# Optimization experiments

Hardware: AMD Instinct MI355X
Metric: run time of the kernel (lower is better)

The kernel has to match this reference:

```python
import jax, jax.numpy as jnp
import numpy as np

EMBED_DIM = 512
NUM_HEADS = 8
HEAD_DIM = EMBED_DIM // NUM_HEADS


def setup_inputs() -> dict:
    key = jax.random.key(0)
    k1, k2, k3, k4, k5, k6 = jax.random.split(key, 6)
    B, S, D = 2, 4096, EMBED_DIM
    scale = 1.0 / np.sqrt(D)
    return {
        "inputs": jax.random.normal(k1, (B, S, D), dtype=jnp.float32),
        "Wq": jax.random.normal(k2, (D, D), dtype=jnp.float32) * scale,
        "Wk": jax.random.normal(k3, (D, D), dtype=jnp.float32) * scale,
        "Wv": jax.random.normal(k4, (D, D), dtype=jnp.float32) * scale,
        "Wc": jax.random.normal(k5, (D, D), dtype=jnp.float32) * scale,
        "bc": jax.random.normal(k6, (D,), dtype=jnp.float32) * 0.01,
    }


def reference(inputs, Wq, Wk, Wv, Wc, bc):
    B, S, D = inputs.shape
    H, Hd = NUM_HEADS, HEAD_DIM

    def split_heads(x):
        # [B,S,D] -> [B,H,S,Hd]
        return x.reshape(B, S, H, Hd).transpose(0, 2, 1, 3)

    # nn.Linear applies x @ W.T
    q = split_heads(inputs @ Wq.T).astype(jnp.float32)
    k = split_heads(inputs @ Wk.T).astype(jnp.float32)
    v = split_heads(inputs @ Wv.T).astype(jnp.float32)

    scores = jnp.einsum("bhqd,bhkd->bhqk", q, k) / np.sqrt(Hd).astype(jnp.float32)
    weights = jax.nn.softmax(scores, axis=-1)
    attended = jnp.einsum("bhqk,bhkd->bhqd", weights, v).astype(inputs.dtype)
    attended = attended.transpose(0, 2, 1, 3).reshape(B, S, D)
    return attended @ Wc.T + bc
```

## Files before the change

### kernel.cpp

```cpp
#include <hip/hip_runtime.h>
#include <cstdint>
#include <cstddef>

typedef _Float16 half_t;
typedef half_t h8 __attribute__((ext_vector_type(8)));
typedef half_t h4 __attribute__((ext_vector_type(4)));
typedef float f4 __attribute__((ext_vector_type(4)));
typedef unsigned int u32;

static constexpr int S_LEN  = 4096;
static constexpr int DMODEL = 512;
static constexpr int NH     = 8;
static constexpr int HD     = 64;
static constexpr int BATCH  = 2;
static constexpr int MTOK   = BATCH * S_LEN;

#define QSCALE 0.18033688011112043f

__device__ __forceinline__ void g2lds16(const void* g, void* l) {
    __builtin_amdgcn_global_load_lds(
        (const __attribute__((address_space(1))) u32*)(uintptr_t)g,
        (__attribute__((address_space(3))) u32*)(u32)(uintptr_t)l,
        16, 0, 0);
}

__device__ __forceinline__ f4 mfma16(h8 a, h8 b, f4 c) {
    return __builtin_amdgcn_mfma_f32_16x16x32_f16(a, b, c, 0, 0, 0);
}

__global__ void cvt_x(const float* __restrict__ in, half_t* __restrict__ out) {
    int i = (blockIdx.x * 256 + threadIdx.x) * 8;
    const float4* p = (const float4*)(in + i);
    float4 a = p[0], b = p[1];
    h8 h;
    h[0]=(half_t)a.x; h[1]=(half_t)a.y; h[2]=(half_t)a.z; h[3]=(half_t)a.w;
    h[4]=(half_t)b.x; h[5]=(half_t)b.y; h[6]=(half_t)b.z; h[7]=(half_t)b.w;
    *(h8*)(out + i) = h;
}

__global__ void cvt_w(const float* __restrict__ w0, const float* __restrict__ w1,
                      const float* __restrict__ w2, const float* __restrict__ w3,
                      half_t* __restrict__ o0, half_t* __restrict__ o1,
                      half_t* __restrict__ o2, half_t* __restrict__ o3) {
    int y = blockIdx.y;
    const float* in = (y==0) ? w0 : (y==1) ? w1 : (y==2) ? w2 : w3;
    half_t* out     = (y==0) ? o0 : (y==1) ? o1 : (y==2) ? o2 : o3;
    float s = (y==0) ? QSCALE : 1.0f;
    int i = (blockIdx.x * 256 + threadIdx.x) * 8;
    const float4* p = (const float4*)(in + i);
    float4 a = p[0], b = p[1];
    h8 h;
    h[0]=(half_t)(a.x*s); h[1]=(half_t)(a.y*s); h[2]=(half_t)(a.z*s); h[3]=(half_t)(a.w*s);
    h[4]=(half_t)(b.x*s); h[5]=(half_t)(b.y*s); h[6]=(half_t)(b.z*s); h[7]=(half_t)(b.w*s);
    *(h8*)(out + i) = h;
}

__device__ __forceinline__ void gemm_core(const half_t* __restrict__ A,
                                          const half_t* __restrict__ B,
                                          int m0, int n0, int Kdim,
                                          half_t* As, half_t* Bs,
                                          f4 (&acc)[4][4]) {
    const int tid  = threadIdx.x;
    const int lane = tid & 63;
    const int w    = tid >> 6;
    const int quad = lane >> 4;
    const int low  = lane & 15;
    const int wr   = (w >> 1) * 64;
    const int wc   = (w & 1) * 64;

    f4 zero = {0.f, 0.f, 0.f, 0.f};
    #pragma unroll
    for (int i = 0; i < 4; ++i)
        #pragma unroll
        for (int j = 0; j < 4; ++j) acc[i][j] = zero;

    for (int kk = 0; kk < Kdim; kk += 32) {
        __syncthreads();
        #pragma unroll
        for (int it = 0; it < 2; ++it) {
            int c = tid + 256 * it;
            int row = c >> 2, cs = c & 3;
            int gc = cs ^ ((row >> 1) & 3);
            g2lds16(A + (size_t)(m0 + row) * Kdim + kk + gc * 8, As + c * 8);
        }
        #pragma unroll
        for (int it = 0; it < 2; ++it) {
            int c = tid + 256 * it;
            int row = c >> 2, cs = c & 3;
            int gc = cs ^ ((row >> 1) & 3);
            g2lds16(B + (size_t)(n0 + row) * Kdim + kk + gc * 8, Bs + c * 8);
        }
        __syncthreads();

        h8 af[4], bf[4];
        #pragma unroll
        for (int i = 0; i < 4; ++i) {
            int r = wr + i * 16 + low;
            af[i] = *(const h8*)(As + r * 32 + (quad ^ ((r >> 1) & 3)) * 8);
        }
        #pragma unroll
        for (int j = 0; j < 4; ++j) {
            int r = wc + j * 16 + low;
            bf[j] = *(const h8*)(Bs + r * 32 + (quad ^ ((r >> 1) & 3)) * 8);
        }
        #pragma unroll
        for (int i = 0; i < 4; ++i)
            #pragma unroll
            for (int j = 0; j < 4; ++j)
                acc[i][j] = mfma16(af[i], bf[j], acc[i][j]);
    }
}

__global__ __launch_bounds__(256) void gemm_qkv(
    const half_t* __restrict__ X,
    const half_t* __restrict__ Wq, const half_t* __restrict__ Wk, const half_t* __restrict__ Wv,
    half_t* __restrict__ Q, half_t* __restrict__ K, half_t* __restrict__ V) {
    __shared__ half_t As[128 * 32];
    __shared__ half_t Bs[128 * 32];
    const int z = blockIdx.z;
    const half_t* W = (z == 0) ? Wq : (z == 1) ? Wk : Wv;
    half_t* O       = (z == 0) ? Q  : (z == 1) ? K  : V;

    const int m0 = blockIdx.y * 128;
    const int n0 = blockIdx.x * 128;
    f4 acc[4][4];
    gemm_core(X, W, m0, n0, DMODEL, As, Bs, acc);

    const int lane = threadIdx.x & 63;
    const int w    = threadIdx.x >> 6;
    const int quad = lane >> 4, low = lane & 15;
    const int wr = (w >> 1) * 64, wc = (w & 1) * 64;

    #pragma unroll
    for (int i = 0; i < 4; ++i) {
        int mb = m0 + wr + i * 16 + quad * 4;
        #pragma unroll
        for (int j = 0; j < 4; ++j) {
            int n = n0 + wc + j * 16 + low;
            int h = n >> 6, d = n & 63;
            #pragma unroll
            for (int r = 0; r < 4; ++r) {
                int m = mb + r;
                int b = m >> 12, s = m & 4095;
                size_t idx = (((size_t)(b * NH + h) << 12) + s) * 64 + d;
                O[idx] = (half_t)acc[i][j][r];
            }
        }
    }
}

__global__ __launch_bounds__(256) void gemm_out(
    const half_t* __restrict__ A, const half_t* __restrict__ W,
    const float* __restrict__ bias, float* __restrict__ out) {
    __shared__ half_t As[128 * 32];
    __shared__ half_t Bs[128 * 32];
    const int m0 = blockIdx.y * 128;
    const int n0 = blockIdx.x * 128;
    f4 acc[4][4];
    gemm_core(A, W, m0, n0, DMODEL, As, Bs, acc);

    const int lane = threadIdx.x & 63;
    const int w    = threadIdx.x >> 6;
    const int quad = lane >> 4, low = lane & 15;
    const int wr = (w >> 1) * 64, wc = (w & 1) * 64;

    #pragma unroll
    for (int i = 0; i < 4; ++i) {
        int mb = m0 + wr + i * 16 + quad * 4;
        #pragma unroll
        for (int j = 0; j < 4; ++j) {
            int n = n0 + wc + j * 16 + low;
            float bv = bias[n];
            #pragma unroll
            for (int r = 0; r < 4; ++r)
                out[(size_t)(mb + r) * DMODEL + n] = acc[i][j][r] + bv;
        }
    }
}

__global__ void transpose_v(const half_t* __restrict__ in, half_t* __restrict__ out) {
    int bh = blockIdx.y;
    int s  = blockIdx.x * 256 + threadIdx.x;
    const half_t* ip = in + ((size_t)bh << 18) + (size_t)s * 64;
    h8 v[8];
    #pragma unroll
    for (int c = 0; c < 8; ++c) v[c] = *(const h8*)(ip + c * 8);
    half_t* op = out + ((size_t)bh << 18) + s;
    #pragma unroll
    for (int d = 0; d < 64; ++d) op[(size_t)d * S_LEN] = v[d >> 3][d & 7];
}

__global__ __launch_bounds__(256, 2) void flash_attn(
    const half_t* __restrict__ Q,
    const half_t* __restrict__ K,
    const half_t* __restrict__ V,
    half_t* __restrict__ Oa) {
    __shared__ half_t Ks[128 * 64];
    __shared__ half_t Vs[64 * 128];
    __shared__ half_t Ps[4 * 32 * 32];

    const int tid  = threadIdx.x;
    const int lane = tid & 63;
    const int w    = tid >> 6;
    const int quad = lane >> 4, low = lane & 15;
    const int bh = blockIdx.y;
    const int q0 = blockIdx.x * 128 + w * 32;

    const half_t* Qb = Q + ((size_t)bh << 18);
    const half_t* Kb = K + ((size_t)bh << 18);
    const half_t* Vb = V + ((size_t)bh << 18);

    h8 qf[2][2];
    #pragma unroll
    for (int i = 0; i < 2; ++i)
        #pragma unroll
        for (int ks = 0; ks < 2; ++ks)
            qf[i][ks] = *(const h8*)(Qb + (size_t)(q0 + i * 16 + low) * 64 + ks * 32 + quad * 8);

    f4 Oacc[2][4];
    f4 zero = {0.f, 0.f, 0.f, 0.f};
    #pragma unroll
    for (int i = 0; i < 2; ++i)
        #pragma unroll
        for (int j = 0; j < 4; ++j) Oacc[i][j] = zero;
    float lrun[2] = {0.f, 0.f};

    half_t* Pw = Ps + w * (32 * 32);

    for (int k0 = 0; k0 < S_LEN; k0 += 128) {
        __syncthreads();
        #pragma unroll
        for (int it = 0; it < 4; ++it) {
            int c = tid + 256 * it;
            int key = c >> 3, cs = c & 7;
            int gc = cs ^ (key & 7);
            g2lds16(Kb + (size_t)(k0 + key) * 64 + gc * 8, Ks + c * 8);
        }
        #pragma unroll
        for (int it = 0; it < 4; ++it) {
            int c = tid + 256 * it;
            int d = c >> 4, cs = c & 15;
            int gc = cs ^ (d & 7);
            g2lds16(Vb + (size_t)d * S_LEN + k0 + gc * 8, Vs + c * 8);
        }
        __syncthreads();

        f4 sc[2][8];
        #pragma unroll
        for (int nt = 0; nt < 8; ++nt) {
            int key = nt * 16 + low;
            h8 kf0 = *(const h8*)(Ks + key * 64 + ((0 + quad) ^ (key & 7)) * 8);
            h8 kf1 = *(const h8*)(Ks + key * 64 + ((4 + quad) ^ (key & 7)) * 8);
            #pragma unroll
            for (int i = 0; i < 2; ++i) {
                sc[i][nt] = mfma16(kf0, qf[i][0], zero);
                sc[i][nt] = mfma16(kf1, qf[i][1], sc[i][nt]);
            }
        }

        #pragma unroll
        for (int i = 0; i < 2; ++i) {
            float rs = 0.f;
            #pragma unroll
            for (int nt = 0; nt < 8; ++nt)
                #pragma unroll
                for (int r = 0; r < 4; ++r) {
                    float p = exp2f(sc[i][nt][r]);
                    sc[i][nt][r] = p;
                    rs += p;
                }
            lrun[i] += rs;
        }

        #pragma unroll
        for (int g = 0; g < 4; ++g) {
            #pragma unroll
            for (int i = 0; i < 2; ++i) {
                int q = i * 16 + low;
                #pragma unroll
                for (int hn = 0; hn < 2; ++hn) {
                    int nt = 2 * g + hn;
                    h4 pk;
                    pk[0] = (half_t)sc[i][nt][0];
                    pk[1] = (half_t)sc[i][nt][1];
                    pk[2] = (half_t)sc[i][nt][2];
                    pk[3] = (half_t)sc[i][nt][3];
                    int cc = (hn * 2 + (quad >> 1)) ^ ((q >> 1) & 3);
                    *(h4*)(Pw + q * 32 + cc * 8 + (quad & 1) * 4) = pk;
                }
            }
            h8 vf[4];
            #pragma unroll
            for (int j = 0; j < 4; ++j) {
                int d = j * 16 + low;
                vf[j] = *(const h8*)(Vs + d * 128 + (((g * 4 + quad)) ^ (d & 7)) * 8);
            }
            h8 pf[2];
            #pragma unroll
            for (int i = 0; i < 2; ++i) {
                int q = i * 16 + low;
                pf[i] = *(const h8*)(Pw + q * 32 + (quad ^ ((q >> 1) & 3)) * 8);
            }
            #pragma unroll
            for (int i = 0; i < 2; ++i)
                #pragma unroll
                for (int j = 0; j < 4; ++j)
                    Oacc[i][j] = mfma16(vf[j], pf[i], Oacc[i][j]);
        }
    }

    #pragma unroll
    for (int i = 0; i < 2; ++i) {
        lrun[i] += __shfl_xor(lrun[i], 16);
        lrun[i] += __shfl_xor(lrun[i], 32);
    }

    const int b = bh >> 3, h = bh & 7;
    #pragma unroll
    for (int i = 0; i < 2; ++i) {
        float inv = 1.0f / lrun[i];
        int qg = q0 + i * 16 + low;
        #pragma unroll
        for (int j = 0; j < 4; ++j) {
            h4 o;
            #pragma unroll
            for (int r = 0; r < 4; ++r) o[r] = (half_t)(Oacc[i][j][r] * inv);
            *(h4*)(Oa + ((size_t)(b * S_LEN + qg)) * DMODEL + h * 64 + j * 16 + quad * 4) = o;
        }
    }
}

extern "C" void kernel_launch(void* const* d_in, const int* in_sizes, int n_in,
                              void* d_out, int out_size, void* d_ws, size_t ws_size,
                              hipStream_t stream) {
    const float* X  = (const float*)d_in[0];
    const float* Wq = (const float*)d_in[1];
    const float* Wk = (const float*)d_in[2];
    const float* Wv = (const float*)d_in[3];
    const float* Wc = (const float*)d_in[4];
    const float* bc = (const float*)d_in[5];
    float* out = (float*)d_out;

    char* ws = (char*)d_ws;
    const size_t SZ_X = (size_t)MTOK * DMODEL * 2;
    const size_t SZ_W = (size_t)DMODEL * DMODEL * 2;
    half_t* Xh   = (half_t*)(ws);
    half_t* Wqh  = (half_t*)(ws + SZ_X);
    half_t* Wkh  = (half_t*)(ws + SZ_X + SZ_W);
    half_t* Wvh  = (half_t*)(ws + SZ_X + 2 * SZ_W);
    half_t* Wch  = (half_t*)(ws + SZ_X + 3 * SZ_W);
    half_t* Qh   = (half_t*)(ws + SZ_X + 4 * SZ_W);
    half_t* Kh   = (half_t*)(ws + 2 * SZ_X + 4 * SZ_W);
    half_t* Vtmp = (half_t*)(ws + 3 * SZ_X + 4 * SZ_W);
    half_t* Vt   = (half_t*)(ws + 4 * SZ_X + 4 * SZ_W);
    half_t* Att  = (half_t*)(ws + 5 * SZ_X + 4 * SZ_W);

    cvt_x<<<2048, 256, 0, stream>>>(X, Xh);
    cvt_w<<<dim3(128, 4), 256, 0, stream>>>(Wq, Wk, Wv, Wc, Wqh, Wkh, Wvh, Wch);
    gemm_qkv<<<dim3(4, 64, 3), 256, 0, stream>>>(Xh, Wqh, Wkh, Wvh, Qh, Kh, Vtmp);
    transpose_v<<<dim3(16, 16), 256, 0, stream>>>(Vtmp, Vt);
    flash_attn<<<dim3(32, 16), 256, 0, stream>>>(Qh, Kh, Vt, Att);
    gemm_out<<<dim3(4, 64), 256, 0, stream>>>(Att, Wch, bc, out);
}
```

Measured before the change: 231.4 us.

## Split attention key range across waves with LDS reduction of partial outputs

Each block now handles 32 queries, and its four waves each process a different 32-key slice of every 128-key chunk. Waves keep private V and P tiles, so the per-iteration block barriers go away. Partial outputs and row sums are combined with a tree reduction through shared memory at the end, and the output is staged through LDS for coalesced stores. The grid grows fourfold and occupancy is raised, at the cost of reloading Q per block, per-wave K loads straight from global memory, and the final reduction overhead.

```diff
diff --git a/kernel.cpp b/kernel.cpp
--- a/kernel.cpp
+++ b/kernel.cpp
@@ -190,143 +190,182 @@
     for (int d = 0; d < 64; ++d) op[(size_t)d * S_LEN] = v[d >> 3][d & 7];
 }
 
-__global__ __launch_bounds__(256, 2) void flash_attn(
+__global__ __launch_bounds__(256, 4) void flash_attn(
     const half_t* __restrict__ Q,
     const half_t* __restrict__ K,
     const half_t* __restrict__ V,
     half_t* __restrict__ Oa) {
-    __shared__ half_t Ks[128 * 64];
-    __shared__ half_t Vs[64 * 128];
-    __shared__ half_t Ps[4 * 32 * 32];
+    __shared__ __align__(16) char smem[24832];
+    half_t* Vs   = (half_t*)smem;
+    half_t* Ps   = (half_t*)(smem + 16384);
+    float*  Ored = (float*)smem;
+    float*  Lred = (float*)(smem + 24576);
 
     const int tid  = threadIdx.x;
     const int lane = tid & 63;
     const int w    = tid >> 6;
     const int quad = lane >> 4, low = lane & 15;
     const int bh = blockIdx.y;
-    const int q0 = blockIdx.x * 128 + w * 32;
+    const int qb = blockIdx.x * 32;
 
     const half_t* Qb = Q + ((size_t)bh << 18);
     const half_t* Kb = K + ((size_t)bh << 18);
     const half_t* Vb = V + ((size_t)bh << 18);
 
+    half_t* Vw = Vs + w * 2048;
+    half_t* Pw = Ps + w * 1024;
+
     h8 qf[2][2];
     #pragma unroll
     for (int i = 0; i < 2; ++i)
         #pragma unroll
         for (int ks = 0; ks < 2; ++ks)
-            qf[i][ks] = *(const h8*)(Qb + (size_t)(q0 + i * 16 + low) * 64 + ks * 32 + quad * 8);
-
-    f4 Oacc[2][4];
+            qf[i][ks] = *(const h8*)(Qb + (size_t)(qb + i * 16 + low) * 64 + ks * 32 + quad * 8);
+
+    f4 Oacc[4][2];
     f4 zero = {0.f, 0.f, 0.f, 0.f};
     #pragma unroll
-    for (int i = 0; i < 2; ++i)
-        #pragma unroll
-        for (int j = 0; j < 4; ++j) Oacc[i][j] = zero;
-    float lrun[2] = {0.f, 0.f};
-
-    half_t* Pw = Ps + w * (32 * 32);
+    for (int j = 0; j < 4; ++j)
+        #pragma unroll
+        for (int i = 0; i < 2; ++i) Oacc[j][i] = zero;
+    float lsum[2] = {0.f, 0.f};
+
+    const int vd = lane >> 2;
+    const int vc = lane & 3;
 
     for (int k0 = 0; k0 < S_LEN; k0 += 128) {
-        __syncthreads();
+        const int kw = k0 + w * 32;
+        asm volatile("s_waitcnt lgkmcnt(0)" ::: "memory");
         #pragma unroll
         for (int it = 0; it < 4; ++it) {
-            int c = tid + 256 * it;
-            int key = c >> 3, cs = c & 7;
-            int gc = cs ^ (key & 7);
-            g2lds16(Kb + (size_t)(k0 + key) * 64 + gc * 8, Ks + c * 8);
-        }
-        #pragma unroll
-        for (int it = 0; it < 4; ++it) {
-            int c = tid + 256 * it;
-            int d = c >> 4, cs = c & 15;
-            int gc = cs ^ (d & 7);
-            g2lds16(Vb + (size_t)d * S_LEN + k0 + gc * 8, Vs + c * 8);
-        }
-        __syncthreads();
-
-        f4 sc[2][8];
-        #pragma unroll
-        for (int nt = 0; nt < 8; ++nt) {
-            int key = nt * 16 + low;
-            h8 kf0 = *(const h8*)(Ks + key * 64 + ((0 + quad) ^ (key & 7)) * 8);
-            h8 kf1 = *(const h8*)(Ks + key * 64 + ((4 + quad) ^ (key & 7)) * 8);
+            int d = it * 16 + vd;
+            int gc = vc ^ (d & 3);
+            g2lds16(Vb + (size_t)d * S_LEN + kw + gc * 8, Vw + it * 512);
+        }
+        h8 kf[2][2];
+        #pragma unroll
+        for (int nt = 0; nt < 2; ++nt)
+            #pragma unroll
+            for (int ks = 0; ks < 2; ++ks)
+                kf[nt][ks] = *(const h8*)(Kb + (size_t)(kw + nt * 16 + low) * 64 + ks * 32 + quad * 8);
+        asm volatile("s_waitcnt vmcnt(0)" ::: "memory");
+
+        f4 sc[2][2];
+        #pragma unroll
+        for (int nt = 0; nt < 2; ++nt)
             #pragma unroll
             for (int i = 0; i < 2; ++i) {
-                sc[i][nt] = mfma16(kf0, qf[i][0], zero);
-                sc[i][nt] = mfma16(kf1, qf[i][1], sc[i][nt]);
+                sc[i][nt] = mfma16(kf[nt][0], qf[i][0], zero);
+                sc[i][nt] = mfma16(kf[nt][1], qf[i][1], sc[i][nt]);
             }
-        }
 
         #pragma unroll
         for (int i = 0; i < 2; ++i) {
-            float rs = 0.f;
-            #pragma unroll
-            for (int nt = 0; nt < 8; ++nt)
+            int q = i * 16 + low;
+            #pragma unroll
+            for (int nt = 0; nt < 2; ++nt) {
+                h4 ph;
                 #pragma unroll
                 for (int r = 0; r < 4; ++r) {
                     float p = exp2f(sc[i][nt][r]);
-                    sc[i][nt][r] = p;
-                    rs += p;
+                    lsum[i] += p;
+                    ph[r] = (half_t)p;
                 }
-            lrun[i] += rs;
-        }
-
-        #pragma unroll
-        for (int g = 0; g < 4; ++g) {
-            #pragma unroll
-            for (int i = 0; i < 2; ++i) {
-                int q = i * 16 + low;
+                int cc = (nt * 2 + (quad >> 1)) ^ ((q >> 1) & 3);
+                *(h4*)(Pw + q * 32 + cc * 8 + (quad & 1) * 4) = ph;
+            }
+        }
+
+        h8 pf[2];
+        #pragma unroll
+        for (int i = 0; i < 2; ++i) {
+            int q = i * 16 + low;
+            pf[i] = *(const h8*)(Pw + q * 32 + (quad ^ ((q >> 1) & 3)) * 8);
+        }
+        #pragma unroll
+        for (int j = 0; j < 4; ++j) {
+            int d = j * 16 + low;
+            h8 vf = *(const h8*)(Vw + d * 32 + (quad ^ (d & 3)) * 8);
+            #pragma unroll
+            for (int i = 0; i < 2; ++i)
+                Oacc[j][i] = mfma16(vf, pf[i], Oacc[j][i]);
+        }
+    }
+
+    #pragma unroll
+    for (int i = 0; i < 2; ++i) {
+        lsum[i] += __shfl_xor(lsum[i], 16);
+        lsum[i] += __shfl_xor(lsum[i], 32);
+    }
+
+    __syncthreads();
+    if (w >= 2) {
+        float* Os = Ored + (w - 2) * 2048;
+        #pragma unroll
+        for (int j = 0; j < 4; ++j)
+            #pragma unroll
+            for (int i = 0; i < 2; ++i)
+                *(f4*)(Os + (j * 2 + i) * 256 + lane * 4) = Oacc[j][i];
+        if (quad == 0) {
+            Lred[(w - 2) * 32 + low]      = lsum[0];
+            Lred[(w - 2) * 32 + 16 + low] = lsum[1];
+        }
+    }
+    __syncthreads();
+    if (w < 2) {
+        float* Os = Ored + w * 2048;
+        #pragma unroll
+        for (int j = 0; j < 4; ++j)
+            #pragma unroll
+            for (int i = 0; i < 2; ++i)
+                Oacc[j][i] += *(const f4*)(Os + (j * 2 + i) * 256 + lane * 4);
+        #pragma unroll
+        for (int i = 0; i < 2; ++i)
+            lsum[i] += Lred[w * 32 + i * 16 + low];
+    }
+    __syncthreads();
+    if (w == 1) {
+        #pragma unroll
+        for (int j = 0; j < 4; ++j)
+            #pragma unroll
+            for (int i = 0; i < 2; ++i)
+                *(f4*)(Ored + (j * 2 + i) * 256 + lane * 4) = Oacc[j][i];
+        if (quad == 0) {
+            Lred[low]      = lsum[0];
+            Lred[16 + low] = lsum[1];
+        }
+    }
+    __syncthreads();
+    if (w == 0) {
+        #pragma unroll
+        for (int j = 0; j < 4; ++j)
+            #pragma unroll
+            for (int i = 0; i < 2; ++i)
+                Oacc[j][i] += *(const f4*)(Ored + (j * 2 + i) * 256 + lane * 4);
+        float inv[2];
+        #pragma unroll
+        for (int i = 0; i < 2; ++i)
+            inv[i] = 1.0f / (lsum[i] + Lred[i * 16 + low]);
+        half_t* Ot = (half_t*)smem;
+        #pragma unroll
+        for (int i = 0; i < 2; ++i) {
+            int q = i * 16 + low;
+            #pragma unroll
+            for (int j = 0; j < 4; ++j) {
+                h4 o;
                 #pragma unroll
-                for (int hn = 0; hn < 2; ++hn) {
-                    int nt = 2 * g + hn;
-                    h4 pk;
-                    pk[0] = (half_t)sc[i][nt][0];
-                    pk[1] = (half_t)sc[i][nt][1];
-                    pk[2] = (half_t)sc[i][nt][2];
-                    pk[3] = (half_t)sc[i][nt][3];
-                    int cc = (hn * 2 + (quad >> 1)) ^ ((q >> 1) & 3);
-                    *(h4*)(Pw + q * 32 + cc * 8 + (quad & 1) * 4) = pk;
-                }
+                for (int r = 0; r < 4; ++r) o[r] = (half_t)(Oacc[j][i][r] * inv[i]);
+                int c = (j * 2 + (quad >> 1)) ^ (q & 7);
+                *(h4*)(Ot + q * 64 + c * 8 + (quad & 1) * 4) = o;
             }
-            h8 vf[4];
-            #pragma unroll
-            for (int j = 0; j < 4; ++j) {
-                int d = j * 16 + low;
-                vf[j] = *(const h8*)(Vs + d * 128 + (((g * 4 + quad)) ^ (d & 7)) * 8);
-            }
-            h8 pf[2];
-            #pragma unroll
-            for (int i = 0; i < 2; ++i) {
-                int q = i * 16 + low;
-                pf[i] = *(const h8*)(Pw + q * 32 + (quad ^ ((q >> 1) & 3)) * 8);
-            }
-            #pragma unroll
-            for (int i = 0; i < 2; ++i)
-                #pragma unroll
-                for (int j = 0; j < 4; ++j)
-                    Oacc[i][j] = mfma16(vf[j], pf[i], Oacc[i][j]);
-        }
-    }
-
-    #pragma unroll
-    for (int i = 0; i < 2; ++i) {
-        lrun[i] += __shfl_xor(lrun[i], 16);
-        lrun[i] += __shfl_xor(lrun[i], 32);
-    }
-
-    const int b = bh >> 3, h = bh & 7;
-    #pragma unroll
-    for (int i = 0; i < 2; ++i) {
-        float inv = 1.0f / lrun[i];
-        int qg = q0 + i * 16 + low;
-        #pragma unroll
-        for (int j = 0; j < 4; ++j) {
-            h4 o;
-            #pragma unroll
-            for (int r = 0; r < 4; ++r) o[r] = (half_t)(Oacc[i][j][r] * inv);
-            *(h4*)(Oa + ((size_t)(b * S_LEN + qg)) * DMODEL + h * 64 + j * 16 + quad * 4) = o;
-        }
+        }
+    }
+    __syncthreads();
+    {
+        int q = tid >> 3, gc = tid & 7;
+        const int b = bh >> 3, h = bh & 7;
+        h8 val = *(const h8*)((const half_t*)smem + q * 64 + ((gc ^ (q & 7)) * 8));
+        *(h8*)(Oa + ((size_t)(b * S_LEN + qb + q)) * DMODEL + h * 64 + gc * 8) = val;
     }
 }
 
@@ -359,6 +398,6 @@
     cvt_w<<<dim3(128, 4), 256, 0, stream>>>(Wq, Wk, Wv, Wc, Wqh, Wkh, Wvh, Wch);
     gemm_qkv<<<dim3(4, 64, 3), 256, 0, stream>>>(Xh, Wqh, Wkh, Wvh, Qh, Kh, Vtmp);
     transpose_v<<<dim3(16, 16), 256, 0, stream>>>(Vtmp, Vt);
-    flash_attn<<<dim3(32, 16), 256, 0, stream>>>(Qh, Kh, Vt, Att);
+    flash_attn<<<dim3(128, 16), 256, 0, stream>>>(Qh, Kh, Vt, Att);
     gemm_out<<<dim3(4, 64), 256, 0, stream>>>(Att, Wch, bc, out);
 }
```

Result: slower. 273.4 us (+18.1%).

## Compute V transposed in GEMM, double-buffer K/V tiles, use fast exp2

Applied to the files above, without the earlier changes.

A new gemm_vt kernel computes Wv·X^T so V comes out directly in the transposed [bh][d][s] layout, which removes the separate transpose kernel and its extra global round trip. Flash attention now double-buffers the K and V LDS tiles, issuing async loads for the next block before computing the current one so load latency overlaps compute. The exp2f call is swapped for the hardware intrinsic. Double buffering doubles LDS use for K/V, which can lower occupancy relative to the launch bound of 2 blocks per CU. gemm_vt's stores are strided along s, which may coalesce less well.

```diff
diff --git a/kernel.cpp b/kernel.cpp
--- a/kernel.cpp
+++ b/kernel.cpp
@@ -113,13 +113,13 @@
 
 __global__ __launch_bounds__(256) void gemm_qkv(
     const half_t* __restrict__ X,
-    const half_t* __restrict__ Wq, const half_t* __restrict__ Wk, const half_t* __restrict__ Wv,
-    half_t* __restrict__ Q, half_t* __restrict__ K, half_t* __restrict__ V) {
+    const half_t* __restrict__ Wq, const half_t* __restrict__ Wk,
+    half_t* __restrict__ Q, half_t* __restrict__ K) {
     __shared__ half_t As[128 * 32];
     __shared__ half_t Bs[128 * 32];
     const int z = blockIdx.z;
-    const half_t* W = (z == 0) ? Wq : (z == 1) ? Wk : Wv;
-    half_t* O       = (z == 0) ? Q  : (z == 1) ? K  : V;
+    const half_t* W = (z == 0) ? Wq : Wk;
+    half_t* O       = (z == 0) ? Q  : K;
 
     const int m0 = blockIdx.y * 128;
     const int n0 = blockIdx.x * 128;
@@ -144,6 +144,38 @@
                 int b = m >> 12, s = m & 4095;
                 size_t idx = (((size_t)(b * NH + h) << 12) + s) * 64 + d;
                 O[idx] = (half_t)acc[i][j][r];
+            }
+        }
+    }
+}
+
+__global__ __launch_bounds__(256) void gemm_vt(
+    const half_t* __restrict__ X, const half_t* __restrict__ Wv,
+    half_t* __restrict__ Vt) {
+    __shared__ half_t As[128 * 32];
+    __shared__ half_t Bs[128 * 32];
+    const int m0 = blockIdx.y * 128;
+    const int n0 = blockIdx.x * 128;
+    f4 acc[4][4];
+    gemm_core(Wv, X, m0, n0, DMODEL, As, Bs, acc);
+
+    const int lane = threadIdx.x & 63;
+    const int w    = threadIdx.x >> 6;
+    const int quad = lane >> 4, low = lane & 15;
+    const int wr = (w >> 1) * 64, wc = (w & 1) * 64;
+
+    #pragma unroll
+    for (int i = 0; i < 4; ++i) {
+        int dgb = m0 + wr + i * 16 + quad * 4;
+        #pragma unroll
+        for (int j = 0; j < 4; ++j) {
+            int tok = n0 + wc + j * 16 + low;
+            int b = tok >> 12, s = tok & 4095;
+            #pragma unroll
+            for (int r = 0; r < 4; ++r) {
+                int dg = dgb + r;
+                size_t idx = (((size_t)(b * NH + (dg >> 6)) << 18)) + ((dg & 63) << 12) + s;
+                Vt[idx] = (half_t)acc[i][j][r];
             }
         }
     }
@@ -178,25 +210,13 @@
     }
 }
 
-__global__ void transpose_v(const half_t* __restrict__ in, half_t* __restrict__ out) {
-    int bh = blockIdx.y;
-    int s  = blockIdx.x * 256 + threadIdx.x;
-    const half_t* ip = in + ((size_t)bh << 18) + (size_t)s * 64;
-    h8 v[8];
-    #pragma unroll
-    for (int c = 0; c < 8; ++c) v[c] = *(const h8*)(ip + c * 8);
-    half_t* op = out + ((size_t)bh << 18) + s;
-    #pragma unroll
-    for (int d = 0; d < 64; ++d) op[(size_t)d * S_LEN] = v[d >> 3][d & 7];
-}
-
 __global__ __launch_bounds__(256, 2) void flash_attn(
     const half_t* __restrict__ Q,
     const half_t* __restrict__ K,
     const half_t* __restrict__ V,
     half_t* __restrict__ Oa) {
-    __shared__ half_t Ks[128 * 64];
-    __shared__ half_t Vs[64 * 128];
+    __shared__ half_t Ks[2][128 * 64];
+    __shared__ half_t Vs[2][64 * 128];
     __shared__ half_t Ps[4 * 32 * 32];
 
     const int tid  = threadIdx.x;
@@ -227,30 +247,38 @@
 
     half_t* Pw = Ps + w * (32 * 32);
 
-    for (int k0 = 0; k0 < S_LEN; k0 += 128) {
-        __syncthreads();
+    auto stage = [&](int k0, int p) {
         #pragma unroll
         for (int it = 0; it < 4; ++it) {
             int c = tid + 256 * it;
             int key = c >> 3, cs = c & 7;
             int gc = cs ^ (key & 7);
-            g2lds16(Kb + (size_t)(k0 + key) * 64 + gc * 8, Ks + c * 8);
+            g2lds16(Kb + (size_t)(k0 + key) * 64 + gc * 8, &Ks[p][c * 8]);
         }
         #pragma unroll
         for (int it = 0; it < 4; ++it) {
             int c = tid + 256 * it;
             int d = c >> 4, cs = c & 15;
             int gc = cs ^ (d & 7);
-            g2lds16(Vb + (size_t)d * S_LEN + k0 + gc * 8, Vs + c * 8);
-        }
+            g2lds16(Vb + (size_t)d * S_LEN + k0 + gc * 8, &Vs[p][c * 8]);
+        }
+    };
+
+    stage(0, 0);
+
+    for (int c = 0; c < S_LEN / 128; ++c) {
         __syncthreads();
+        if (c + 1 < S_LEN / 128) stage((c + 1) * 128, (c + 1) & 1);
+
+        const half_t* Kc = Ks[c & 1];
+        const half_t* Vc = Vs[c & 1];
 
         f4 sc[2][8];
         #pragma unroll
         for (int nt = 0; nt < 8; ++nt) {
             int key = nt * 16 + low;
-            h8 kf0 = *(const h8*)(Ks + key * 64 + ((0 + quad) ^ (key & 7)) * 8);
-            h8 kf1 = *(const h8*)(Ks + key * 64 + ((4 + quad) ^ (key & 7)) * 8);
+            h8 kf0 = *(const h8*)(Kc + key * 64 + ((0 + quad) ^ (key & 7)) * 8);
+            h8 kf1 = *(const h8*)(Kc + key * 64 + ((4 + quad) ^ (key & 7)) * 8);
             #pragma unroll
             for (int i = 0; i < 2; ++i) {
                 sc[i][nt] = mfma16(kf0, qf[i][0], zero);
@@ -265,7 +293,7 @@
             for (int nt = 0; nt < 8; ++nt)
                 #pragma unroll
                 for (int r = 0; r < 4; ++r) {
-                    float p = exp2f(sc[i][nt][r]);
+                    float p = __builtin_amdgcn_exp2f(sc[i][nt][r]);
                     sc[i][nt][r] = p;
                     rs += p;
                 }
@@ -293,7 +321,7 @@
             #pragma unroll
             for (int j = 0; j < 4; ++j) {
                 int d = j * 16 + low;
-                vf[j] = *(const h8*)(Vs + d * 128 + (((g * 4 + quad)) ^ (d & 7)) * 8);
+                vf[j] = *(const h8*)(Vc + d * 128 + (((g * 4 + quad)) ^ (d & 7)) * 8);
             }
             h8 pf[2];
             #pragma unroll
@@ -351,14 +379,13 @@
     half_t* Wch  = (half_t*)(ws + SZ_X + 3 * SZ_W);
     half_t* Qh   = (half_t*)(ws + SZ_X + 4 * SZ_W);
     half_t* Kh   = (half_t*)(ws + 2 * SZ_X + 4 * SZ_W);
-    half_t* Vtmp = (half_t*)(ws + 3 * SZ_X + 4 * SZ_W);
-    half_t* Vt   = (half_t*)(ws + 4 * SZ_X + 4 * SZ_W);
-    half_t* Att  = (half_t*)(ws + 5 * SZ_X + 4 * SZ_W);
+    half_t* Vt   = (half_t*)(ws + 3 * SZ_X + 4 * SZ_W);
+    half_t* Att  = (half_t*)(ws + 4 * SZ_X + 4 * SZ_W);
 
     cvt_x<<<2048, 256, 0, stream>>>(X, Xh);
     cvt_w<<<dim3(128, 4), 256, 0, stream>>>(Wq, Wk, Wv, Wc, Wqh, Wkh, Wvh, Wch);
-    gemm_qkv<<<dim3(4, 64, 3), 256, 0, stream>>>(Xh, Wqh, Wkh, Wvh, Qh, Kh, Vtmp);
-    transpose_v<<<dim3(16, 16), 256, 0, stream>>>(Vtmp, Vt);
+    gemm_qkv<<<dim3(4, 64, 2), 256, 0, stream>>>(Xh, Wqh, Wkh, Qh, Kh);
+    gemm_vt<<<dim3(64, 4), 256, 0, stream>>>(Xh, Wvh, Vt);
     flash_attn<<<dim3(32, 16), 256, 0, stream>>>(Qh, Kh, Vt, Att);
     gemm_out<<<dim3(4, 64), 256, 0, stream>>>(Att, Wch, bc, out);
 }
```

Measured after the change: 204.9 us. 1.13x faster.
